# Kernel optimization log

Measured on AMD Instinct MI355X. Metric: run time of the kernel, lower is better.

## Reference

```python
import jax, jax.numpy as jnp
import numpy as np

N_NODES = 100352
NUM_GRAPHS = 512
NODES_PER_GRAPH = 196  # N_NODES / NUM_GRAPHS, equal-size graphs
N_EDGES = 1605632
IN_C, HID_C, OUT_C, K = 128, 64, 32, 30


def setup_inputs() -> dict:
    key = jax.random.key(0)
    ks = jax.random.split(key, 4)
    x = jax.random.normal(ks[0], (N_NODES, IN_C), dtype=jnp.float32)
    edge_index = jax.random.randint(ks[1], (2, N_EDGES), 0, N_NODES, dtype=jnp.int32)
    batch = jnp.repeat(jnp.arange(NUM_GRAPHS, dtype=jnp.int32), NODES_PER_GRAPH)
    W1 = jax.random.normal(ks[2], (IN_C, HID_C), jnp.float32) * (1.0 / np.sqrt(IN_C))
    b1 = jnp.zeros((HID_C,), jnp.float32)
    W2 = jax.random.normal(ks[3], (HID_C, OUT_C), jnp.float32) * (1.0 / np.sqrt(HID_C))
    b2 = jnp.zeros((OUT_C,), jnp.float32)
    return dict(x=x, edge_index=edge_index, batch=batch, W1=W1, b1=b1, W2=W2, b2=b2)


def gcn_conv(x, src, dst, W, b, num_nodes):
    # PyG GCNConv: xW, add self-loops, symmetric normalization, scatter-add to dst.
    xw = x @ W  # [N, D_out]
    deg = jax.ops.segment_sum(jnp.ones_like(dst, dtype=xw.dtype), dst,
                              num_segments=num_nodes) + 1.0  # +1 for self-loop
    dis = jax.lax.rsqrt(deg)  # deg^{-1/2}
    msg = (dis[src] * dis[dst])[:, None] * xw[src]  # [E, D_out]
    out = jax.ops.segment_sum(msg, dst, num_segments=num_nodes)
    out = out + (dis * dis)[:, None] * xw  # self-loop term deg^{-1} * xw
    return out + b


def sort_pool(x, batch, num_graphs, max_nodes, k):
    # PyG SortAggregation: dense per-graph batch, sort nodes desc by last channel, top-k, zero padding.
    N, D = x.shape
    fill = x.min() - 1.0
    counts = jax.ops.segment_sum(jnp.ones((N,), jnp.int32), batch, num_segments=num_graphs)
    starts = jnp.cumsum(counts) - counts  # exclusive prefix sum
    pos = jnp.arange(N, dtype=jnp.int32) - starts[batch]
    dense = jnp.full((num_graphs, max_nodes, D), fill, x.dtype).at[batch, pos].set(x)
    order = jnp.argsort(-dense[:, :, -1], axis=1)[:, :k]  # [B, k] top-k by last channel
    topk = jnp.take_along_axis(dense, order[:, :, None], axis=1)  # [B, k, D]
    topk = jnp.where(topk == fill, jnp.zeros((), x.dtype), topk)
    return topk.reshape(num_graphs, k * D)


def reference(x, edge_index, batch, W1, b1, W2, b2):
    src, dst = edge_index[0], edge_index[1]
    n = x.shape[0]
    h = jax.nn.relu(gcn_conv(x, src, dst, W1, b1, n))
    h = gcn_conv(h, src, dst, W2, b2, n)
    return sort_pool(h, batch, NUM_GRAPHS, NODES_PER_GRAPH, K)
```

## Files before the change

kernel.cpp:

```cpp
#include <hip/hip_runtime.h>

#define N_NODES   100352
#define N_EDGES   1605632
#define IN_C      128
#define HID_C     64
#define OUT_C     32
#define NUM_GRAPHS 512
#define NPG       196
#define TOPK      30

#define NB        196
#define BCAP      10240
#define LCAP      10240

typedef float v16f __attribute__((ext_vector_type(16)));

#define OFF_DEG     0u
#define OFF_ROWPTR  401408u
#define OFF_DIS     802816u
#define OFF_BCNT    1204224u
#define OFF_BBASE   1205248u
#define OFF_ARENA   1206272u
#define OFF_OUT2    1206272u
#define OFF_CSR     17262592u
#define OFF_XW1     23685120u
#define OFF_XW2     75065344u

__global__ __launch_bounds__(256) void k_bucket(const int* __restrict__ src, const int* __restrict__ dst,
                                                int* __restrict__ bucket_cnt, int* __restrict__ arena) {
    __shared__ int hist[NB];
    __shared__ int cur[NB];
    int tid = threadIdx.x;
    for (int i = tid; i < NB; i += 256) hist[i] = 0;
    __syncthreads();
    int e0 = (blockIdx.x * 256 + tid) * 8;
    int4 sa = ((const int4*)src)[e0 / 4], sb = ((const int4*)src)[e0 / 4 + 1];
    int4 da = ((const int4*)dst)[e0 / 4], db = ((const int4*)dst)[e0 / 4 + 1];
    int es[8] = {sa.x, sa.y, sa.z, sa.w, sb.x, sb.y, sb.z, sb.w};
    int ed[8] = {da.x, da.y, da.z, da.w, db.x, db.y, db.z, db.w};
    int eb[8];
#pragma unroll
    for (int j = 0; j < 8; ++j) { eb[j] = ed[j] >> 9; atomicAdd(&hist[eb[j]], 1); }
    __syncthreads();
    for (int i = tid; i < NB; i += 256) {
        int c = hist[i];
        cur[i] = (c > 0) ? atomicAdd(&bucket_cnt[i], c) : 0;
    }
    __syncthreads();
#pragma unroll
    for (int j = 0; j < 8; ++j) {
        int p = atomicAdd(&cur[eb[j]], 1);
        if (p < BCAP) arena[(size_t)eb[j] * BCAP + p] = (es[j] << 9) | (ed[j] & 511);
    }
}

__global__ __launch_bounds__(256) void k_bscan(const int* __restrict__ bucket_cnt, int* __restrict__ bucket_base) {
    __shared__ int s[256];
    int t = threadIdx.x;
    int v = (t < NB) ? bucket_cnt[t] : 0;
    s[t] = v;
    __syncthreads();
    for (int o = 1; o < 256; o <<= 1) {
        int a = (t >= o) ? s[t - o] : 0;
        __syncthreads();
        s[t] += a;
        __syncthreads();
    }
    if (t < NB) bucket_base[t] = s[t] - v;
}

__global__ __launch_bounds__(256) void k_build(const int* __restrict__ arena, const int* __restrict__ bucket_cnt,
                                               const int* __restrict__ bucket_base, int* __restrict__ row_ptr,
                                               int* __restrict__ deg, float* __restrict__ dis,
                                               int* __restrict__ csr_src) {
    __shared__ int dloc[512];
    __shared__ int sc[512];
    __shared__ int cur[512];
    __shared__ int stage[LCAP];
    int b = blockIdx.x;
    int tid = threadIdx.x;
    int nb = min(bucket_cnt[b], BCAP);
    int gbase = bucket_base[b];
    const int* ap = arena + (size_t)b * BCAP;
    for (int i = tid; i < 512; i += 256) dloc[i] = 0;
    __syncthreads();
    for (int i = tid; i < nb; i += 256) {
        int e = ap[i];
        atomicAdd(&dloc[e & 511], 1);
    }
    __syncthreads();
    for (int i = tid; i < 512; i += 256) sc[i] = dloc[i];
    __syncthreads();
    for (int o = 1; o < 512; o <<= 1) {
        int i0 = tid, i1 = tid + 256;
        int v0 = (i0 >= o) ? sc[i0 - o] : 0;
        int v1 = (i1 >= o) ? sc[i1 - o] : 0;
        __syncthreads();
        sc[i0] += v0;
        sc[i1] += v1;
        __syncthreads();
    }
    for (int i = tid; i < 512; i += 256) {
        int d = dloc[i];
        int off = sc[i] - d;
        int node = b * 512 + i;
        row_ptr[node] = gbase + off;
        deg[node] = d;
        dis[node] = (float)(1.0 / sqrt((double)(d + 1)));
        cur[i] = off;
    }
    __syncthreads();
    bool inlds = (nb <= LCAP);
    for (int i = tid; i < nb; i += 256) {
        int e = ap[i];
        int p = atomicAdd(&cur[e & 511], 1);
        int sv = ((unsigned)e) >> 9;
        if (inlds) stage[p] = sv;
        else       csr_src[gbase + p] = sv;
    }
    __syncthreads();
    if (inlds)
        for (int i = tid; i < nb; i += 256) csr_src[gbase + i] = stage[i];
}

__global__ __launch_bounds__(256) void k_mm1(const float* __restrict__ x, const float* __restrict__ W1,
                                             const float* __restrict__ dis, float* __restrict__ xw1s) {
    int tid = threadIdx.x;
    int n = blockIdx.x * 64 + (tid & 63);
    int ch = __builtin_amdgcn_readfirstlane((tid >> 6) * 16);
    const float4* xrow = (const float4*)(x + (size_t)n * IN_C);
    float acc[16];
#pragma unroll
    for (int c = 0; c < 16; ++c) acc[c] = 0.f;
    float4 xq = xrow[0];
#pragma unroll 1
    for (int q = 0; q < IN_C / 4; ++q) {
        float4 xn = xrow[(q + 1) & (IN_C / 4 - 1)];
        const float* wp = W1 + q * 4 * HID_C + ch;
        v16f w0, w1, w2, w3;
        asm volatile("s_load_dwordx16 %0, %1, 0x0"   : "=s"(w0) : "s"(wp));
        asm volatile("s_load_dwordx16 %0, %1, 0x100" : "=s"(w1) : "s"(wp));
        asm volatile("s_load_dwordx16 %0, %1, 0x200" : "=s"(w2) : "s"(wp));
        asm volatile("s_load_dwordx16 %0, %1, 0x300" : "=s"(w3) : "s"(wp));
        asm volatile("s_waitcnt lgkmcnt(0)" : "+s"(w0), "+s"(w1), "+s"(w2), "+s"(w3));
#pragma unroll
        for (int c = 0; c < 16; ++c) {
            acc[c] = fmaf(xq.x, w0[c], acc[c]);
            acc[c] = fmaf(xq.y, w1[c], acc[c]);
            acc[c] = fmaf(xq.z, w2[c], acc[c]);
            acc[c] = fmaf(xq.w, w3[c], acc[c]);
        }
        xq = xn;
    }
    float dv = dis[n];
    float4* orow = (float4*)(xw1s + (size_t)n * HID_C + ch);
#pragma unroll
    for (int c4 = 0; c4 < 4; ++c4) {
        float4 o;
        o.x = acc[4 * c4 + 0] * dv;
        o.y = acc[4 * c4 + 1] * dv;
        o.z = acc[4 * c4 + 2] * dv;
        o.w = acc[4 * c4 + 3] * dv;
        orow[c4] = o;
    }
}

__global__ __launch_bounds__(256) void k_agg1(const float* __restrict__ xw1s, const int* __restrict__ csr_src,
                                              const int* __restrict__ row_ptr, const int* __restrict__ deg,
                                              const float* __restrict__ dis, const float* __restrict__ b1,
                                              const float* __restrict__ W2, float* __restrict__ xw2s) {
    __shared__ float w2lds[HID_C * OUT_C];
    int tid = threadIdx.x;
    for (int i = tid; i < HID_C * OUT_C / 4; i += 256)
        ((float4*)w2lds)[i] = ((const float4*)W2)[i];
    __syncthreads();
    int lane = tid & 63;
    int v = blockIdx.x * 4 + (tid >> 6);
    int start = row_ptr[v];
    int cnt = deg[v];
    float acc0 = xw1s[(size_t)v * HID_C + lane];
    float acc1 = 0.f, acc2 = 0.f, acc3 = 0.f;
    for (int base = 0; base < cnt; base += 64) {
        int mcnt = min(64, cnt - base);
        int sj = 0;
        if (lane < mcnt) sj = csr_src[start + base + lane];
        int j = 0;
        for (; j + 8 <= mcnt; j += 8) {
            int s0 = __shfl(sj, j + 0), s1 = __shfl(sj, j + 1);
            int s2 = __shfl(sj, j + 2), s3 = __shfl(sj, j + 3);
            int s4 = __shfl(sj, j + 4), s5 = __shfl(sj, j + 5);
            int s6 = __shfl(sj, j + 6), s7 = __shfl(sj, j + 7);
            float v0 = xw1s[(size_t)s0 * HID_C + lane];
            float v1 = xw1s[(size_t)s1 * HID_C + lane];
            float v2 = xw1s[(size_t)s2 * HID_C + lane];
            float v3 = xw1s[(size_t)s3 * HID_C + lane];
            float v4 = xw1s[(size_t)s4 * HID_C + lane];
            float v5 = xw1s[(size_t)s5 * HID_C + lane];
            float v6 = xw1s[(size_t)s6 * HID_C + lane];
            float v7 = xw1s[(size_t)s7 * HID_C + lane];
            acc0 += v0 + v4;
            acc1 += v1 + v5;
            acc2 += v2 + v6;
            acc3 += v3 + v7;
        }
        for (; j < mcnt; ++j) {
            int s = __shfl(sj, j);
            acc0 += xw1s[(size_t)s * HID_C + lane];
        }
    }
    float dv = dis[v];
    float o = fmaf(dv, (acc0 + acc1) + (acc2 + acc3), b1[lane]);
    float hval = fmaxf(o, 0.f);

    int c = lane & 31;
    int hf = lane & 32;
    float s = 0.f;
#pragma unroll
    for (int k0 = 0; k0 < 32; ++k0) {
        float hk = __shfl(hval, k0 | hf);
        s = fmaf(hk, w2lds[((k0 | hf) << 5) + c], s);
    }
    s += __shfl_xor(s, 32);
    if (lane < 32)
        xw2s[(size_t)v * OUT_C + c] = s * dv;
}

__global__ __launch_bounds__(256) void k_agg2(const float* __restrict__ xw2s, const int* __restrict__ csr_src,
                                              const int* __restrict__ row_ptr, const int* __restrict__ deg,
                                              const float* __restrict__ dis, const float* __restrict__ b2,
                                              float* __restrict__ out2) {
    int lane = threadIdx.x & 31;
    int v = blockIdx.x * 8 + (threadIdx.x >> 5);
    int start = row_ptr[v];
    int cnt = deg[v];
    float acc0 = xw2s[(size_t)v * OUT_C + lane];
    float acc1 = 0.f, acc2 = 0.f, acc3 = 0.f;
    for (int base = 0; base < cnt; base += 32) {
        int mcnt = min(32, cnt - base);
        int sj = 0;
        if (lane < mcnt) sj = csr_src[start + base + lane];
        int j = 0;
        for (; j + 8 <= mcnt; j += 8) {
            int s0 = __shfl(sj, j + 0, 32), s1 = __shfl(sj, j + 1, 32);
            int s2 = __shfl(sj, j + 2, 32), s3 = __shfl(sj, j + 3, 32);
            int s4 = __shfl(sj, j + 4, 32), s5 = __shfl(sj, j + 5, 32);
            int s6 = __shfl(sj, j + 6, 32), s7 = __shfl(sj, j + 7, 32);
            float v0 = xw2s[(size_t)s0 * OUT_C + lane];
            float v1 = xw2s[(size_t)s1 * OUT_C + lane];
            float v2 = xw2s[(size_t)s2 * OUT_C + lane];
            float v3 = xw2s[(size_t)s3 * OUT_C + lane];
            float v4 = xw2s[(size_t)s4 * OUT_C + lane];
            float v5 = xw2s[(size_t)s5 * OUT_C + lane];
            float v6 = xw2s[(size_t)s6 * OUT_C + lane];
            float v7 = xw2s[(size_t)s7 * OUT_C + lane];
            acc0 += v0 + v4;
            acc1 += v1 + v5;
            acc2 += v2 + v6;
            acc3 += v3 + v7;
        }
        for (; j < mcnt; ++j) {
            int s = __shfl(sj, j, 32);
            acc0 += xw2s[(size_t)s * OUT_C + lane];
        }
    }
    out2[(size_t)v * OUT_C + lane] = fmaf(dis[v], (acc0 + acc1) + (acc2 + acc3), b2[lane]);
}

__global__ __launch_bounds__(256) void k_sort(const float* __restrict__ out2, float* __restrict__ out) {
    __shared__ float keys[NPG];
    __shared__ int order[TOPK];
    int g = blockIdx.x;
    int tid = threadIdx.x;
    int base = g * NPG;
    if (tid < NPG) keys[tid] = out2[(size_t)(base + tid) * OUT_C + (OUT_C - 1)];
    __syncthreads();
    if (tid < NPG) {
        float my = keys[tid];
        int r = 0;
        for (int j = 0; j < NPG; ++j) {
            float kj = keys[j];
            r += (kj > my) || (kj == my && j < tid);
        }
        if (r < TOPK) order[r] = tid;
    }
    __syncthreads();
    for (int idx = tid; idx < TOPK * OUT_C; idx += 256) {
        int r = idx >> 5;
        int c = idx & 31;
        int n = order[r];
        out[g * (TOPK * OUT_C) + idx] = out2[(size_t)(base + n) * OUT_C + c];
    }
}

extern "C" void kernel_launch(void* const* d_in, const int* in_sizes, int n_in,
                              void* d_out, int out_size, void* d_ws, size_t ws_size,
                              hipStream_t stream) {
    const float* x  = (const float*)d_in[0];
    const int*   ei = (const int*)d_in[1];
    const int*   srcp = ei;
    const int*   dstp = ei + N_EDGES;
    const float* W1 = (const float*)d_in[3];
    const float* b1 = (const float*)d_in[4];
    const float* W2 = (const float*)d_in[5];
    const float* b2 = (const float*)d_in[6];
    float* out = (float*)d_out;

    char* w = (char*)d_ws;
    int*    deg      = (int*)(w + OFF_DEG);
    int*    row_ptr  = (int*)(w + OFF_ROWPTR);
    float*  dis      = (float*)(w + OFF_DIS);
    int*    bcnt     = (int*)(w + OFF_BCNT);
    int*    bbase    = (int*)(w + OFF_BBASE);
    int*    arena    = (int*)(w + OFF_ARENA);
    int*    csr_src  = (int*)(w + OFF_CSR);
    float*  xw1s     = (float*)(w + OFF_XW1);
    float*  xw2s     = (float*)(w + OFF_XW2);
    float*  out2     = (float*)(w + OFF_OUT2);

    hipMemsetAsync(bcnt, 0, NB * sizeof(int), stream);
    k_bucket<<<N_EDGES / (256 * 8), 256, 0, stream>>>(srcp, dstp, bcnt, arena);
    k_bscan <<<1, 256, 0, stream>>>(bcnt, bbase);
    k_build <<<NB, 256, 0, stream>>>(arena, bcnt, bbase, row_ptr, deg, dis, csr_src);
    k_mm1   <<<N_NODES / 64, 256, 0, stream>>>(x, W1, dis, xw1s);
    k_agg1  <<<N_NODES / 4, 256, 0, stream>>>(xw1s, csr_src, row_ptr, deg, dis, b1, W2, xw2s);
    k_agg2  <<<N_NODES / 8, 256, 0, stream>>>(xw2s, csr_src, row_ptr, deg, dis, b2, out2);
    k_sort  <<<NUM_GRAPHS, 256, 0, stream>>>(out2, out);
}
```

Measured before the change: 226.5 us.

## Fold bucket scan into build kernel and split layer-2 matmul out of agg1

The single-block bucket prefix-scan kernel is removed. Each build block now redundantly scans the 196 bucket counts itself, which saves one launch and a dependency. The W2 projection is taken out of the aggregation kernel: agg1 now writes the hidden activations h to memory, and a new scalar-load matmul kernel (k_mm2) computes h·W2 scaled by deg^{-1/2}. This drops the LDS staging and the shuffle-based matmul from the gather kernel, at the cost of one extra launch and a write plus re-read of the 100352x64 h buffer.

```diff
diff --git a/kernel.cpp b/kernel.cpp
--- a/kernel.cpp
+++ b/kernel.cpp
@@ -19,11 +19,11 @@
 #define OFF_ROWPTR  401408u
 #define OFF_DIS     802816u
 #define OFF_BCNT    1204224u
-#define OFF_BBASE   1205248u
 #define OFF_ARENA   1206272u
 #define OFF_OUT2    1206272u
 #define OFF_CSR     17262592u
 #define OFF_XW1     23685120u
+#define OFF_H       49375232u
 #define OFF_XW2     75065344u
 
 __global__ __launch_bounds__(256) void k_bucket(const int* __restrict__ src, const int* __restrict__ dst,
@@ -54,33 +54,28 @@
     }
 }
 
-__global__ __launch_bounds__(256) void k_bscan(const int* __restrict__ bucket_cnt, int* __restrict__ bucket_base) {
-    __shared__ int s[256];
-    int t = threadIdx.x;
-    int v = (t < NB) ? bucket_cnt[t] : 0;
-    s[t] = v;
-    __syncthreads();
-    for (int o = 1; o < 256; o <<= 1) {
-        int a = (t >= o) ? s[t - o] : 0;
-        __syncthreads();
-        s[t] += a;
-        __syncthreads();
-    }
-    if (t < NB) bucket_base[t] = s[t] - v;
-}
-
 __global__ __launch_bounds__(256) void k_build(const int* __restrict__ arena, const int* __restrict__ bucket_cnt,
-                                               const int* __restrict__ bucket_base, int* __restrict__ row_ptr,
+                                               int* __restrict__ row_ptr,
                                                int* __restrict__ deg, float* __restrict__ dis,
                                                int* __restrict__ csr_src) {
+    __shared__ int bsc[256];
     __shared__ int dloc[512];
     __shared__ int sc[512];
     __shared__ int cur[512];
     __shared__ int stage[LCAP];
     int b = blockIdx.x;
     int tid = threadIdx.x;
+    int bv = (tid < NB) ? bucket_cnt[tid] : 0;
+    bsc[tid] = bv;
+    __syncthreads();
+    for (int o = 1; o < 256; o <<= 1) {
+        int a = (tid >= o) ? bsc[tid - o] : 0;
+        __syncthreads();
+        bsc[tid] += a;
+        __syncthreads();
+    }
     int nb = min(bucket_cnt[b], BCAP);
-    int gbase = bucket_base[b];
+    int gbase = bsc[b] - bucket_cnt[b];
     const int* ap = arena + (size_t)b * BCAP;
     for (int i = tid; i < 512; i += 256) dloc[i] = 0;
     __syncthreads();
@@ -168,14 +163,9 @@
 __global__ __launch_bounds__(256) void k_agg1(const float* __restrict__ xw1s, const int* __restrict__ csr_src,
                                               const int* __restrict__ row_ptr, const int* __restrict__ deg,
                                               const float* __restrict__ dis, const float* __restrict__ b1,
-                                              const float* __restrict__ W2, float* __restrict__ xw2s) {
-    __shared__ float w2lds[HID_C * OUT_C];
-    int tid = threadIdx.x;
-    for (int i = tid; i < HID_C * OUT_C / 4; i += 256)
-        ((float4*)w2lds)[i] = ((const float4*)W2)[i];
-    __syncthreads();
-    int lane = tid & 63;
-    int v = blockIdx.x * 4 + (tid >> 6);
+                                              float* __restrict__ h) {
+    int lane = threadIdx.x & 63;
+    int v = blockIdx.x * 4 + (threadIdx.x >> 6);
     int start = row_ptr[v];
     int cnt = deg[v];
     float acc0 = xw1s[(size_t)v * HID_C + lane];
@@ -208,21 +198,50 @@
             acc0 += xw1s[(size_t)s * HID_C + lane];
         }
     }
-    float dv = dis[v];
-    float o = fmaf(dv, (acc0 + acc1) + (acc2 + acc3), b1[lane]);
-    float hval = fmaxf(o, 0.f);
-
-    int c = lane & 31;
-    int hf = lane & 32;
-    float s = 0.f;
-#pragma unroll
-    for (int k0 = 0; k0 < 32; ++k0) {
-        float hk = __shfl(hval, k0 | hf);
-        s = fmaf(hk, w2lds[((k0 | hf) << 5) + c], s);
-    }
-    s += __shfl_xor(s, 32);
-    if (lane < 32)
-        xw2s[(size_t)v * OUT_C + c] = s * dv;
+    float o = fmaf(dis[v], (acc0 + acc1) + (acc2 + acc3), b1[lane]);
+    h[(size_t)v * HID_C + lane] = fmaxf(o, 0.f);
+}
+
+__global__ __launch_bounds__(256) void k_mm2(const float* __restrict__ h, const float* __restrict__ W2,
+                                             const float* __restrict__ dis, float* __restrict__ xw2s) {
+    int tid = threadIdx.x;
+    int n = blockIdx.x * 128 + (tid & 127);
+    int ch = __builtin_amdgcn_readfirstlane((tid >> 7) * 16);
+    const float4* hrow = (const float4*)(h + (size_t)n * HID_C);
+    float acc[16];
+#pragma unroll
+    for (int c = 0; c < 16; ++c) acc[c] = 0.f;
+    float4 xq = hrow[0];
+#pragma unroll 1
+    for (int q = 0; q < HID_C / 4; ++q) {
+        float4 xn = hrow[(q + 1) & (HID_C / 4 - 1)];
+        const float* wp = W2 + q * 4 * OUT_C + ch;
+        v16f w0, w1, w2, w3;
+        asm volatile("s_load_dwordx16 %0, %1, 0x0"   : "=s"(w0) : "s"(wp));
+        asm volatile("s_load_dwordx16 %0, %1, 0x80"  : "=s"(w1) : "s"(wp));
+        asm volatile("s_load_dwordx16 %0, %1, 0x100" : "=s"(w2) : "s"(wp));
+        asm volatile("s_load_dwordx16 %0, %1, 0x180" : "=s"(w3) : "s"(wp));
+        asm volatile("s_waitcnt lgkmcnt(0)" : "+s"(w0), "+s"(w1), "+s"(w2), "+s"(w3));
+#pragma unroll
+        for (int c = 0; c < 16; ++c) {
+            acc[c] = fmaf(xq.x, w0[c], acc[c]);
+            acc[c] = fmaf(xq.y, w1[c], acc[c]);
+            acc[c] = fmaf(xq.z, w2[c], acc[c]);
+            acc[c] = fmaf(xq.w, w3[c], acc[c]);
+        }
+        xq = xn;
+    }
+    float dv = dis[n];
+    float4* orow = (float4*)(xw2s + (size_t)n * OUT_C + ch);
+#pragma unroll
+    for (int c4 = 0; c4 < 4; ++c4) {
+        float4 o;
+        o.x = acc[4 * c4 + 0] * dv;
+        o.y = acc[4 * c4 + 1] * dv;
+        o.z = acc[4 * c4 + 2] * dv;
+        o.w = acc[4 * c4 + 3] * dv;
+        orow[c4] = o;
+    }
 }
 
 __global__ __launch_bounds__(256) void k_agg2(const float* __restrict__ xw2s, const int* __restrict__ csr_src,
@@ -310,19 +329,19 @@
     int*    row_ptr  = (int*)(w + OFF_ROWPTR);
     float*  dis      = (float*)(w + OFF_DIS);
     int*    bcnt     = (int*)(w + OFF_BCNT);
-    int*    bbase    = (int*)(w + OFF_BBASE);
     int*    arena    = (int*)(w + OFF_ARENA);
     int*    csr_src  = (int*)(w + OFF_CSR);
     float*  xw1s     = (float*)(w + OFF_XW1);
+    float*  h        = (float*)(w + OFF_H);
     float*  xw2s     = (float*)(w + OFF_XW2);
     float*  out2     = (float*)(w + OFF_OUT2);
 
     hipMemsetAsync(bcnt, 0, NB * sizeof(int), stream);
     k_bucket<<<N_EDGES / (256 * 8), 256, 0, stream>>>(srcp, dstp, bcnt, arena);
-    k_bscan <<<1, 256, 0, stream>>>(bcnt, bbase);
-    k_build <<<NB, 256, 0, stream>>>(arena, bcnt, bbase, row_ptr, deg, dis, csr_src);
+    k_build <<<NB, 256, 0, stream>>>(arena, bcnt, row_ptr, deg, dis, csr_src);
     k_mm1   <<<N_NODES / 64, 256, 0, stream>>>(x, W1, dis, xw1s);
-    k_agg1  <<<N_NODES / 4, 256, 0, stream>>>(xw1s, csr_src, row_ptr, deg, dis, b1, W2, xw2s);
+    k_agg1  <<<N_NODES / 4, 256, 0, stream>>>(xw1s, csr_src, row_ptr, deg, dis, b1, h);
+    k_mm2   <<<N_NODES / 128, 256, 0, stream>>>(h, W2, dis, xw2s);
     k_agg2  <<<N_NODES / 8, 256, 0, stream>>>(xw2s, csr_src, row_ptr, deg, dis, b2, out2);
     k_sort  <<<NUM_GRAPHS, 256, 0, stream>>>(out2, out);
 }
```

After: 220.7 us. 1.03x faster.
